# Optimization experiments

Hardware: AMD Instinct MI355X
Metric: run time of the kernel (lower is better)

Reference implementation:

```python
import jax, jax.numpy as jnp
import numpy as np

C = 1024
FACTOR = 4
C_INT = C * FACTOR


def setup_inputs() -> dict:
    key = jax.random.key(0)
    ks = jax.random.split(key, 6)
    act = jax.random.normal(ks[0], (4, 2048, C), dtype=jnp.float32)
    mask = jnp.ones((4, 2048), dtype=jnp.float32)
    # LayerNorm params
    ln_scale = jnp.ones((C,), dtype=jnp.float32)
    ln_bias = jnp.zeros((C,), dtype=jnp.float32)
    # Linear 1 (init='linear'): lecun-normal-ish
    w1 = jax.random.normal(ks[1], (C, C_INT), dtype=jnp.float32) / np.sqrt(C)
    b1 = jnp.zeros((C_INT,), dtype=jnp.float32)
    # Linear 2 (init='final' -> zeros in AF2; use small random so grads are nontrivial)
    w2 = jax.random.normal(ks[2], (C_INT, C), dtype=jnp.float32) * 0.02
    b2 = jnp.zeros((C,), dtype=jnp.float32)
    return {"act": act, "mask": mask, "ln_scale": ln_scale, "ln_bias": ln_bias,
            "w1": w1, "b1": b1, "w2": w2, "b2": b2}


def _layernorm(x, scale, bias, eps=1e-5):
    mu = jnp.mean(x, axis=-1, keepdims=True)
    var = jnp.mean(jnp.square(x - mu), axis=-1, keepdims=True)
    return (x - mu) * jax.lax.rsqrt(var + eps) * scale + bias


def reference(act, mask, ln_scale, ln_bias, w1, b1, w2, b2):
    # mask is accepted but unused, matching the original forward.
    x = _layernorm(act, ln_scale, ln_bias)
    h = jax.nn.relu(jnp.einsum('bsc,cf->bsf', x, w1) + b1)
    return jnp.einsum('bsf,fc->bsc', h, w2) + b2
```

## Files before the change

### kernel.cpp

```cpp
#include <hip/hip_runtime.h>
#include <hip/hip_bf16.h>
#include <cstdint>

typedef unsigned short u16;
typedef __bf16 bf16x8 __attribute__((ext_vector_type(8)));
typedef float floatx4 __attribute__((ext_vector_type(4)));

#define AS1 __attribute__((address_space(1)))
#define AS3 __attribute__((address_space(3)))

static __device__ __forceinline__ u16 f2bf(float f) {
    union { float f; unsigned int u; } v; v.f = f;
    unsigned int u = v.u;
    return (u16)((u + 0x7FFFu + ((u >> 16) & 1u)) >> 16);
}

__device__ __forceinline__ void transpose_body(
    const float* __restrict__ in, u16* __restrict__ out,
    int R, int Ccols, int bx, int by, int tid, float (*tile)[33])
{
    const int tx = tid & 31;
    const int ty = tid >> 5;
    const int c0 = bx * 32;
    const int r0 = by * 32;
#pragma unroll
    for (int i = 0; i < 32; i += 8)
        tile[ty + i][tx] = in[(size_t)(r0 + ty + i) * Ccols + (c0 + tx)];
    __syncthreads();
#pragma unroll
    for (int i = 0; i < 32; i += 8)
        out[(size_t)(c0 + ty + i) * R + (r0 + tx)] = f2bf(tile[tx][ty + i]);
}

__global__ __launch_bounds__(256)
void prep(const float* __restrict__ w1, const float* __restrict__ w2,
          const float* __restrict__ act, const float* __restrict__ ln_scale,
          const float* __restrict__ ln_bias,
          u16* __restrict__ W1t, u16* __restrict__ W2t, u16* __restrict__ X)
{
    __shared__ float smem[32][33];
    const int id  = blockIdx.x;
    const int tid = threadIdx.x;

    if (id < 4096) {
        transpose_body(w1, W1t, 1024, 4096, id & 127, id >> 7, tid, smem);
        return;
    }
    if (id < 8192) {
        const int t = id - 4096;
        transpose_body(w2, W2t, 4096, 1024, t & 31, t >> 5, tid, smem);
        return;
    }
    const int row = id - 8192;
    const float4 v = ((const float4*)(act + (size_t)row * 1024))[tid];
    float s  = v.x + v.y + v.z + v.w;
    float ss = v.x * v.x + v.y * v.y + v.z * v.z + v.w * v.w;
#pragma unroll
    for (int off = 32; off > 0; off >>= 1) {
        s  += __shfl_xor(s, off, 64);
        ss += __shfl_xor(ss, off, 64);
    }
    float* red = &smem[0][0];
    const int wave = tid >> 6, lane = tid & 63;
    if (lane == 0) { red[wave] = s; red[4 + wave] = ss; }
    __syncthreads();
    s  = red[0] + red[1] + red[2] + red[3];
    ss = red[4] + red[5] + red[6] + red[7];
    const float mu  = s * (1.0f / 1024.0f);
    const float var = ss * (1.0f / 1024.0f) - mu * mu;
    const float rs  = rsqrtf(var + 1e-5f);
    const float4 sc = ((const float4*)ln_scale)[tid];
    const float4 bi = ((const float4*)ln_bias)[tid];
    ushort4 o;
    o.x = f2bf((v.x - mu) * rs * sc.x + bi.x);
    o.y = f2bf((v.y - mu) * rs * sc.y + bi.y);
    o.z = f2bf((v.z - mu) * rs * sc.z + bi.z);
    o.w = f2bf((v.w - mu) * rs * sc.w + bi.w);
    ((ushort4*)(X + (size_t)row * 1024))[tid] = o;
}

template <int BK, bool BF16_OUT, bool RELU>
__global__ __launch_bounds__(256)
void gemm_bt(const u16* __restrict__ A,
             const u16* __restrict__ Bt,
             const float* __restrict__ bias,
             void* __restrict__ Cout,
             int M, int N, int K)
{
    constexpr int SLOTS  = BK / 8;
    constexpr int RPI    = 64 / SLOTS;
    constexpr int IPW    = SLOTS / 2;
    constexpr int HALVES = BK / 32;

    __shared__ __align__(16) u16 Alds[128 * BK];
    __shared__ __align__(16) u16 Blds[128 * BK];

    const int tid  = threadIdx.x;
    const int wave = tid >> 6;
    const int lane = tid & 63;
    const int wm   = wave & 1;
    const int wn   = wave >> 1;
    const int quad = lane >> 4;
    const int l16  = lane & 15;

    const int nbn = N >> 7;
    const int id  = blockIdx.x;
    const int grp = id / (8 * nbn);
    const int rem = id - grp * 8 * nbn;
    const int bm  = grp * 8 + (rem & 7);
    const int bn  = rem >> 3;

    const u16* Ag = A  + (size_t)bm * 128 * K;
    const u16* Bg = Bt + (size_t)bn * 128 * K;

    const int srow = lane / SLOTS;
    const int s_st = lane & (SLOTS - 1);
    const int s_g  = (SLOTS == 4) ? (s_st ^ ((srow >> 1) & 3))
                                  : (s_st ^ (srow & 7));
    const int scol = s_g * 8;

    const int rkey = (SLOTS == 4) ? ((l16 >> 1) & 3) : (l16 & 7);

    floatx4 acc[4][4];
#pragma unroll
    for (int i = 0; i < 4; ++i)
#pragma unroll
        for (int j = 0; j < 4; ++j)
            acc[i][j] = (floatx4){0.f, 0.f, 0.f, 0.f};

    for (int k0 = 0; k0 < K; k0 += BK) {
        __syncthreads();
#pragma unroll
        for (int r = 0; r < IPW; ++r) {
            const int chunk = wave * IPW + r;
            const int row = chunk * RPI + srow;
            __builtin_amdgcn_global_load_lds(
                (AS1 void*)(Ag + (size_t)row * K + k0 + scol),
                (AS3 void*)(&Alds[chunk * 512]), 16, 0, 0);
            __builtin_amdgcn_global_load_lds(
                (AS1 void*)(Bg + (size_t)row * K + k0 + scol),
                (AS3 void*)(&Blds[chunk * 512]), 16, 0, 0);
        }
        __syncthreads();

#pragma unroll
        for (int h = 0; h < HALVES; ++h) {
            const int slot = ((quad + 4 * h) ^ rkey) * 8;
            bf16x8 bfr[4];
#pragma unroll
            for (int ni = 0; ni < 4; ++ni) {
                const int brow = wn * 64 + ni * 16 + l16;
                bfr[ni] = *(const bf16x8*)(&Blds[brow * BK + slot]);
            }
#pragma unroll
            for (int mi = 0; mi < 4; ++mi) {
                const int arow = wm * 64 + mi * 16 + l16;
                const bf16x8 a = *(const bf16x8*)(&Alds[arow * BK + slot]);
#pragma unroll
                for (int ni = 0; ni < 4; ++ni)
                    acc[mi][ni] = __builtin_amdgcn_mfma_f32_16x16x32_bf16(
                        bfr[ni], a, acc[mi][ni], 0, 0, 0);
            }
        }
    }

    const int mbase = bm * 128 + wm * 64;
    const int nbase = bn * 128 + wn * 64;
#pragma unroll
    for (int mi = 0; mi < 4; ++mi) {
        const int m = mbase + mi * 16 + l16;
#pragma unroll
        for (int ni = 0; ni < 4; ++ni) {
            const int n0 = nbase + ni * 16 + quad * 4;
            const float4 bv = *(const float4*)&bias[n0];
            float v0 = acc[mi][ni][0] + bv.x;
            float v1 = acc[mi][ni][1] + bv.y;
            float v2 = acc[mi][ni][2] + bv.z;
            float v3 = acc[mi][ni][3] + bv.w;
            if (RELU) {
                v0 = fmaxf(v0, 0.f); v1 = fmaxf(v1, 0.f);
                v2 = fmaxf(v2, 0.f); v3 = fmaxf(v3, 0.f);
            }
            if (BF16_OUT) {
                ushort4 o = { f2bf(v0), f2bf(v1), f2bf(v2), f2bf(v3) };
                *(ushort4*)&((u16*)Cout)[(size_t)m * N + n0] = o;
            } else {
                float4 o = { v0, v1, v2, v3 };
                *(float4*)&((float*)Cout)[(size_t)m * N + n0] = o;
            }
        }
    }
}

extern "C" void kernel_launch(void* const* d_in, const int* in_sizes, int n_in,
                              void* d_out, int out_size, void* d_ws, size_t ws_size,
                              hipStream_t stream)
{
    const float* act      = (const float*)d_in[0];
    const float* ln_scale = (const float*)d_in[2];
    const float* ln_bias  = (const float*)d_in[3];
    const float* w1       = (const float*)d_in[4];
    const float* b1       = (const float*)d_in[5];
    const float* w2       = (const float*)d_in[6];
    const float* b2       = (const float*)d_in[7];
    float* out = (float*)d_out;

    const int M = 8192, C = 1024, CI = 4096;

    u16* X   = (u16*)d_ws;
    u16* W1t = X   + (size_t)M * C;
    u16* W2t = W1t + (size_t)CI * C;
    u16* H   = W2t + (size_t)C * CI;

    prep<<<16384, 256, 0, stream>>>(w1, w2, act, ln_scale, ln_bias, W1t, W2t, X);
    gemm_bt<64, true, true><<<(M / 128) * (CI / 128), 256, 0, stream>>>(
        X, W1t, b1, (void*)H, M, CI, C);
    gemm_bt<64, false, false><<<(M / 128) * (C / 128), 256, 0, stream>>>(
        H, W2t, b2, (void*)out, M, C, CI);
}
```

Measured before the change: 282.0 us.

## Split-K the second GEMM with atomic accumulation and change tile order

The second GEMM (K=4096, only 512 output tiles) is split into two K halves, so twice as many workgroups run. Each half adds its partial result into an output buffer zeroed by memset, using float atomics; only split 0 adds the bias. The block-to-tile mapping also changes from a grouped swizzle to a plain column-major order for both GEMMs. This costs an extra memset pass, atomic traffic on 32MB of output, nondeterministic summation order, and possibly worse L2 reuse in the first GEMM without the swizzle.

```diff
diff --git a/kernel.cpp b/kernel.cpp
--- a/kernel.cpp
+++ b/kernel.cpp
@@ -79,7 +79,7 @@
     ((ushort4*)(X + (size_t)row * 1024))[tid] = o;
 }
 
-template <int BK, bool BF16_OUT, bool RELU>
+template <int BK, int SPLITK, bool BF16_OUT, bool RELU>
 __global__ __launch_bounds__(256)
 void gemm_bt(const u16* __restrict__ A,
              const u16* __restrict__ Bt,
@@ -103,12 +103,16 @@
     const int quad = lane >> 4;
     const int l16  = lane & 15;
 
+    const int nbm = M >> 7;
     const int nbn = N >> 7;
-    const int id  = blockIdx.x;
-    const int grp = id / (8 * nbn);
-    const int rem = id - grp * 8 * nbn;
-    const int bm  = grp * 8 + (rem & 7);
-    const int bn  = rem >> 3;
+    int id = blockIdx.x;
+    const int s   = (SPLITK > 1) ? id / (nbm * nbn) : 0;
+    if (SPLITK > 1) id -= s * nbm * nbn;
+    const int bm  = id % nbm;
+    const int bn  = id / nbm;
+    const int Ks   = K / SPLITK;
+    const int kbeg = s * Ks;
+    const int kend = kbeg + Ks;
 
     const u16* Ag = A  + (size_t)bm * 128 * K;
     const u16* Bg = Bt + (size_t)bn * 128 * K;
@@ -128,7 +132,7 @@
         for (int j = 0; j < 4; ++j)
             acc[i][j] = (floatx4){0.f, 0.f, 0.f, 0.f};
 
-    for (int k0 = 0; k0 < K; k0 += BK) {
+    for (int k0 = kbeg; k0 < kend; k0 += BK) {
         __syncthreads();
 #pragma unroll
         for (int r = 0; r < IPW; ++r) {
@@ -166,6 +170,7 @@
 
     const int mbase = bm * 128 + wm * 64;
     const int nbase = bn * 128 + wn * 64;
+    const bool add_bias = (SPLITK == 1) || (s == 0);
 #pragma unroll
     for (int mi = 0; mi < 4; ++mi) {
         const int m = mbase + mi * 16 + l16;
@@ -173,15 +178,18 @@
         for (int ni = 0; ni < 4; ++ni) {
             const int n0 = nbase + ni * 16 + quad * 4;
             const float4 bv = *(const float4*)&bias[n0];
-            float v0 = acc[mi][ni][0] + bv.x;
-            float v1 = acc[mi][ni][1] + bv.y;
-            float v2 = acc[mi][ni][2] + bv.z;
-            float v3 = acc[mi][ni][3] + bv.w;
+            float v0 = acc[mi][ni][0], v1 = acc[mi][ni][1];
+            float v2 = acc[mi][ni][2], v3 = acc[mi][ni][3];
+            if (add_bias) { v0 += bv.x; v1 += bv.y; v2 += bv.z; v3 += bv.w; }
             if (RELU) {
                 v0 = fmaxf(v0, 0.f); v1 = fmaxf(v1, 0.f);
                 v2 = fmaxf(v2, 0.f); v3 = fmaxf(v3, 0.f);
             }
-            if (BF16_OUT) {
+            if (SPLITK > 1) {
+                float* p = &((float*)Cout)[(size_t)m * N + n0];
+                atomicAdd(p + 0, v0); atomicAdd(p + 1, v1);
+                atomicAdd(p + 2, v2); atomicAdd(p + 3, v3);
+            } else if (BF16_OUT) {
                 ushort4 o = { f2bf(v0), f2bf(v1), f2bf(v2), f2bf(v3) };
                 *(ushort4*)&((u16*)Cout)[(size_t)m * N + n0] = o;
             } else {
@@ -212,9 +220,10 @@
     u16* W2t = W1t + (size_t)CI * C;
     u16* H   = W2t + (size_t)C * CI;
 
+    hipMemsetAsync(out, 0, (size_t)M * C * sizeof(float), stream);
     prep<<<16384, 256, 0, stream>>>(w1, w2, act, ln_scale, ln_bias, W1t, W2t, X);
-    gemm_bt<64, true, true><<<(M / 128) * (CI / 128), 256, 0, stream>>>(
+    gemm_bt<64, 1, true, true><<<(M / 128) * (CI / 128), 256, 0, stream>>>(
         X, W1t, b1, (void*)H, M, CI, C);
-    gemm_bt<64, false, false><<<(M / 128) * (C / 128), 256, 0, stream>>>(
+    gemm_bt<64, 2, false, false><<<(M / 128) * (C / 128) * 2, 256, 0, stream>>>(
         H, W2t, b2, (void*)out, M, C, CI);
 }
```

Measured after the change: 469.8 us. 66.6% more time.
